# Performance work log

Hardware: AMD Instinct MI355X
Metric: run time of the kernel (lower is better)

## Reference

```python
import jax, jax.numpy as jnp
import numpy as np
from jax.scipy.special import erfc

# Problem scale
B, N, K = 16, 4000, 64          # systems, atoms/system, max neighbors
L = 30.0                         # cubic cell edge (Angstrom)
ALPHA = 0.3                      # Ewald splitting parameter (1/A), from config
KCUT = 1.0                       # reciprocal-space cutoff (1/A), from config
NMAX = 4                         # floor(KCUT / (2*pi/L)) -> static k-grid half-width
COULOMB_CONSTANT = 14.399645351950548  # e^2/(4 pi eps0) in eV*A


def setup_inputs() -> dict:
    key = jax.random.key(0)
    k1, k2, k3, k4 = jax.random.split(key, 4)
    T = B * N
    positions = jax.random.uniform(k1, (T, 3), dtype=jnp.float32) * L
    node_charges = jax.random.normal(k2, (T,), dtype=jnp.float32)
    cell = jnp.tile(jnp.eye(3, dtype=jnp.float32) * L, (B, 1, 1))
    # neighbor indices restricted to the same system; -1 marks self/padding
    local = jax.random.randint(k3, (T, K), 0, N)
    base = (jnp.arange(T) // N) * N
    nm = local + base[:, None]
    nm = jnp.where(nm == jnp.arange(T)[:, None], -1, nm).astype(jnp.int32)
    neighbor_shifts = jnp.zeros((T, K, 3), dtype=jnp.int32)
    num_neighbors = jnp.full((T,), K, dtype=jnp.int32)
    batch_idx = (jnp.arange(T) // N).astype(jnp.int32)
    return dict(positions=positions, node_charges=node_charges, cell=cell,
                neighbor_matrix=nm, neighbor_shifts=neighbor_shifts,
                num_neighbors=num_neighbors, batch_idx=batch_idx)


def _ewald_energies(positions, node_charges, cell, neighbor_matrix,
                    neighbor_shifts, num_neighbors, batch_idx):
    T = positions.shape[0]
    Bn = cell.shape[0]
    Nn = T // Bn
    Kn = neighbor_matrix.shape[1]
    q = node_charges.reshape(-1)
    dtype = positions.dtype
    alpha = jnp.full((Bn,), ALPHA, dtype=dtype)
    a_i = alpha[batch_idx]                                  # [T]

    # ---- real-space: neighbor gather + erfc + scatter-less per-atom sum ----
    mask = (neighbor_matrix >= 0) & (jnp.arange(Kn)[None, :] < num_neighbors[:, None])
    j = jnp.where(mask, neighbor_matrix, 0)                 # safe gather index [T,K]
    off = jnp.einsum('tks,tsd->tkd', neighbor_shifts.astype(dtype), cell[batch_idx])
    rij = positions[j] + off - positions[:, None, :]        # [T,K,3]
    d = jnp.sqrt(jnp.where(mask, jnp.sum(rij * rij, -1), 1.0))
    pair = jnp.where(mask, q[:, None] * q[j] * erfc(a_i[:, None] * d) / d, 0.0)
    # 0.5 for full (non-half) neighbor list; Gaussian self-interaction correction
    e_real = 0.5 * jnp.sum(pair, axis=-1) - a_i / jnp.sqrt(jnp.pi) * q * q  # [T]

    # ---- reciprocal-space: structure-factor sum over k-vectors ----
    rng = np.arange(-NMAX, NMAX + 1)
    nvec = np.stack(np.meshgrid(rng, rng, rng, indexing='ij'), -1).reshape(-1, 3)
    nvec = jnp.asarray(nvec, dtype=dtype)                   # [G,3] integer grid
    recip = 2.0 * jnp.pi * jnp.transpose(jnp.linalg.inv(cell), (0, 2, 1))  # rows b_j
    kv = jnp.einsum('gj,bjd->bgd', nvec, recip)             # [B,G,3]
    k2 = jnp.sum(kv * kv, -1)                               # [B,G]
    kmask = (k2 > 1e-10) & (k2 <= KCUT * KCUT)
    vol = jnp.abs(jnp.linalg.det(cell))                     # [B]
    a2 = alpha * alpha
    coef = jnp.where(kmask,
                     4.0 * jnp.pi * jnp.exp(-k2 / (4.0 * a2[:, None])) / jnp.where(kmask, k2, 1.0),
                     0.0) / (2.0 * vol[:, None])            # [B,G]
    pos_b = positions.reshape(Bn, Nn, 3)
    q_b = q.reshape(Bn, Nn)
    phase = jnp.einsum('bnd,bgd->bng', pos_b, kv)           # [B,N,G]
    c = jnp.cos(phase)
    s = jnp.sin(phase)
    Sre = jnp.einsum('bn,bng->bg', q_b, c)
    Sim = jnp.einsum('bn,bng->bg', q_b, s)
    e_recip = q_b * (jnp.einsum('bng,bg->bn', c, coef * Sre) +
                     jnp.einsum('bng,bg->bn', s, coef * Sim))  # [B,N]

    per_atom = e_real + e_recip.reshape(-1)
    energies = jax.ops.segment_sum(per_atom, batch_idx, num_segments=Bn)
    return energies * COULOMB_CONSTANT


def reference(positions, node_charges, cell, neighbor_matrix, neighbor_shifts,
              num_neighbors, batch_idx):
    return _ewald_energies(positions, node_charges, cell, neighbor_matrix,
                           neighbor_shifts, num_neighbors, batch_idx)
```

## Files before the change

### kernel.cpp

```cpp
#include <hip/hip_runtime.h>
#include <math.h>

#define GPB    8
#define GTOT   729
#define GMAX   46
#define KMAX   (GMAX*GPB)
#define APB    16
#define STRIDE 344

__device__ __forceinline__ float wave_reduce(float v) {
    #pragma unroll
    for (int off = 32; off > 0; off >>= 1) v += __shfl_down(v, off, 64);
    return v;
}

__device__ __forceinline__ float fast_erfc(float x) {
    float t = __builtin_amdgcn_rcpf(fmaf(0.3275911f, x, 1.0f));
    float p = fmaf(1.061405429f, t, -1.453152027f);
    p = fmaf(p, t, 1.421413741f);
    p = fmaf(p, t, -0.284496736f);
    p = fmaf(p, t, 0.254829592f);
    return p * t * __expf(-x * x);
}

__global__ __launch_bounds__(256)
void pack_pq(const float* __restrict__ pos, const float* __restrict__ chg,
             float4* __restrict__ pq, int T)
{
    int t = blockIdx.x * 256 + threadIdx.x;
    if (t < T)
        pq[t] = make_float4(pos[3*t], pos[3*t+1], pos[3*t+2], chg[t]);
}

__global__ __launch_bounds__(64)
void build_kvecs(const float* __restrict__ cell, float4* __restrict__ kcomp,
                 int* __restrict__ kcnt)
{
    const float TWO_PI = 6.283185307179586f;
    const float INV4A2 = 2.7777777777f;
    const float KC2    = 1.0f;

    int b    = blockIdx.x;
    int lane = threadIdx.x;

    const float* C = cell + 9 * b;
    float m00=C[0], m01=C[1], m02=C[2];
    float m10=C[3], m11=C[4], m12=C[5];
    float m20=C[6], m21=C[7], m22=C[8];
    float a00 = m11*m22 - m12*m21;
    float a01 = m02*m21 - m01*m22;
    float a02 = m01*m12 - m02*m11;
    float a10 = m12*m20 - m10*m22;
    float a11 = m00*m22 - m02*m20;
    float a12 = m02*m10 - m00*m12;
    float a20 = m10*m21 - m11*m20;
    float a21 = m01*m20 - m00*m21;
    float a22 = m00*m11 - m01*m10;
    float det = m00*a00 + m01*a10 + m02*a20;
    float invdet = 1.0f / det;
    float vol = fabsf(det);

    int cnt = 0;
    for (int base = 0; base < GTOT; base += 64) {
        int g = base + lane;
        float kx = 0.f, ky = 0.f, kz = 0.f, cf = 0.f;
        if (g < GTOT) {
            int ix = g / 81, rem = g - ix * 81;
            int iy = rem / 9, iz = rem - iy * 9;
            int nx = ix - 4, ny = iy - 4, nz = iz - 4;
            bool pos_half = (nx > 0) || (nx == 0 && (ny > 0 || (ny == 0 && nz > 0)));
            if (pos_half) {
                float fx = (float)nx, fy = (float)ny, fz = (float)nz;
                kx = TWO_PI * invdet * (fx*a00 + fy*a01 + fz*a02);
                ky = TWO_PI * invdet * (fx*a10 + fy*a11 + fz*a12);
                kz = TWO_PI * invdet * (fx*a20 + fy*a21 + fz*a22);
                float k2 = kx*kx + ky*ky + kz*kz;
                if (k2 > 1e-10f && k2 <= KC2) {
                    cf = 12.566370614359172f * __expf(-k2 * INV4A2) / (k2 * vol);
                }
            }
        }
        bool act = (cf != 0.f);
        unsigned long long m = __ballot(act);
        if (act) {
            int off = __popcll(m & ((1ull << lane) - 1ull));
            kcomp[b * KMAX + cnt + off] = make_float4(kx, ky, kz, cf);
        }
        cnt += (int)__popcll(m);
    }
    int padded = ((cnt + GPB - 1) / GPB) * GPB;
    if (lane < padded - cnt)
        kcomp[b * KMAX + cnt + lane] = make_float4(0.f, 0.f, 0.f, 0.f);
    if (lane == 0) kcnt[b] = padded / GPB;
}

__global__ __launch_bounds__(256)
void ewald_fused2(const float4* __restrict__ pq,
                  const float*  __restrict__ cell,
                  const int*    __restrict__ nm,
                  const int*    __restrict__ shifts,
                  const int*    __restrict__ nnb,
                  const float4* __restrict__ kcomp,
                  const int*    __restrict__ kcnt,
                  float* __restrict__ partial,
                  int T, int N, int K, int Bn, int CB)
{
    __shared__ float4 skv[GPB];
    __shared__ float  redA[4][GPB];
    __shared__ float  redB[4][GPB];
    __shared__ float  redr[4];

    const float ALPHA       = 0.3f;
    const float INV_SQRT_PI = 0.5641895835477563f;

    int blk  = blockIdx.x;
    int lane = threadIdx.x & 63;
    int w    = threadIdx.x >> 6;

    if (blk < CB) {
        int b    = blk / GMAX;
        int grp  = blk - b * GMAX;
        int slot = b * STRIDE + (N / APB) + grp;
        int ng   = kcnt[b];
        if (grp >= ng) {
            if (threadIdx.x == 0) partial[slot] = 0.f;
            return;
        }

        if (threadIdx.x < GPB)
            skv[threadIdx.x] = kcomp[b * KMAX + grp * GPB + threadIdx.x];
        __syncthreads();

        float kvx[GPB], kvy[GPB], kvz[GPB];
        #pragma unroll
        for (int gi = 0; gi < GPB; ++gi) {
            float4 v = skv[gi];
            kvx[gi] = v.x; kvy[gi] = v.y; kvz[gi] = v.z;
        }

        float Sre[GPB], Sim[GPB];
        #pragma unroll
        for (int gi = 0; gi < GPB; ++gi) { Sre[gi] = 0.f; Sim[gi] = 0.f; }

        const float4* pb = pq + (size_t)b * N;
        int a = threadIdx.x;
        for (; a + 256 < N; a += 512) {
            float4 v0 = pb[a];
            float4 v1 = pb[a + 256];
            #pragma unroll
            for (int gi = 0; gi < GPB; ++gi) {
                float ph0 = fmaf(v0.x, kvx[gi], fmaf(v0.y, kvy[gi], v0.z * kvz[gi]));
                float ph1 = fmaf(v1.x, kvx[gi], fmaf(v1.y, kvy[gi], v1.z * kvz[gi]));
                float s0, c0, s1, c1;
                __sincosf(ph0, &s0, &c0);
                __sincosf(ph1, &s1, &c1);
                Sre[gi] = fmaf(v0.w, c0, Sre[gi]);
                Sim[gi] = fmaf(v0.w, s0, Sim[gi]);
                Sre[gi] = fmaf(v1.w, c1, Sre[gi]);
                Sim[gi] = fmaf(v1.w, s1, Sim[gi]);
            }
        }
        if (a < N) {
            float4 v0 = pb[a];
            #pragma unroll
            for (int gi = 0; gi < GPB; ++gi) {
                float ph0 = fmaf(v0.x, kvx[gi], fmaf(v0.y, kvy[gi], v0.z * kvz[gi]));
                float s0, c0;
                __sincosf(ph0, &s0, &c0);
                Sre[gi] = fmaf(v0.w, c0, Sre[gi]);
                Sim[gi] = fmaf(v0.w, s0, Sim[gi]);
            }
        }

        #pragma unroll
        for (int gi = 0; gi < GPB; ++gi) {
            float sr = wave_reduce(Sre[gi]);
            float si = wave_reduce(Sim[gi]);
            if (lane == 0) { redA[w][gi] = sr; redB[w][gi] = si; }
        }
        __syncthreads();
        if (threadIdx.x < 64) {
            float e = 0.f;
            if (threadIdx.x < GPB) {
                int gi = threadIdx.x;
                float SR = redA[0][gi] + redA[1][gi] + redA[2][gi] + redA[3][gi];
                float SI = redB[0][gi] + redB[1][gi] + redB[2][gi] + redB[3][gi];
                e = skv[gi].w * (SR * SR + SI * SI);
            }
            e = wave_reduce(e);
            if (threadIdx.x == 0) partial[slot] = e;
        }
    } else {
        int rb = blk - CB;
        int t0 = rb * APB;
        int sys = t0 / N;

        float val = 0.0f;
        #pragma unroll
        for (int i = 0; i < APB/4; ++i) {
            int t = t0 + w * (APB/4) + i;
            float4 vi = pq[t];
            float xi = vi.x, yi = vi.y, zi = vi.z, qi = vi.w;
            if (lane == 0) val -= ALPHA * INV_SQRT_PI * qi * qi;
            int nn = nnb[t];
            for (int k = lane; k < K; k += 64) {
                int p = t * K + k;
                int j = nm[p];
                bool msk = (j >= 0) && (k < nn);
                if (msk) {
                    int sx = shifts[3*p], sy = shifts[3*p+1], sz = shifts[3*p+2];
                    float ox = 0.f, oy = 0.f, oz = 0.f;
                    if ((sx | sy | sz) != 0) {
                        const float* C = cell + 9 * sys;
                        float fx = (float)sx, fy = (float)sy, fz = (float)sz;
                        ox = fx*C[0] + fy*C[3] + fz*C[6];
                        oy = fx*C[1] + fy*C[4] + fz*C[7];
                        oz = fx*C[2] + fy*C[5] + fz*C[8];
                    }
                    float4 vj = pq[j];
                    float dx = vj.x + ox - xi;
                    float dy = vj.y + oy - yi;
                    float dz = vj.z + oz - zi;
                    float r2 = fmaf(dx, dx, fmaf(dy, dy, dz*dz));
                    float rinv = rsqrtf(r2);
                    float d = r2 * rinv;
                    val += 0.5f * qi * vj.w * fast_erfc(ALPHA * d) * rinv;
                }
            }
        }

        val = wave_reduce(val);
        if (lane == 0) redr[w] = val;
        __syncthreads();
        if (threadIdx.x == 0) {
            int rb_in_sys = rb - sys * (N / APB);
            partial[sys * STRIDE + rb_in_sys] =
                redr[0] + redr[1] + redr[2] + redr[3];
        }
    }
}

template <bool PACKED>
__global__ __launch_bounds__(256)
void ewald_fused(const float4* __restrict__ pq,
                 const float*  __restrict__ pos,
                 const float*  __restrict__ chg,
                 const float*  __restrict__ cell,
                 const int*    __restrict__ nm,
                 const int*    __restrict__ shifts,
                 const int*    __restrict__ nnb,
                 float* __restrict__ partial,
                 int T, int N, int K, int Bn, int CB)
{
    __shared__ float red[16];

    const float TWO_PI  = 6.283185307179586f;
    const float ALPHA   = 0.3f;
    const float INV4A2  = 2.7777777777f;
    const float KC2     = 1.0f;
    const float INV_SQRT_PI = 0.5641895835477563f;

    int blk = blockIdx.x;

    if (blk < CB) {
        int gpb_groups = (GTOT + GPB - 1) / GPB;
        int b   = blk / gpb_groups;
        int grp = blk % gpb_groups;

        const float* C = cell + 9 * b;
        float m00=C[0], m01=C[1], m02=C[2];
        float m10=C[3], m11=C[4], m12=C[5];
        float m20=C[6], m21=C[7], m22=C[8];
        float a00 = m11*m22 - m12*m21;
        float a01 = m02*m21 - m01*m22;
        float a02 = m01*m12 - m02*m11;
        float a10 = m12*m20 - m10*m22;
        float a11 = m00*m22 - m02*m20;
        float a12 = m02*m10 - m00*m12;
        float a20 = m10*m21 - m11*m20;
        float a21 = m01*m20 - m00*m21;
        float a22 = m00*m11 - m01*m10;
        float det = m00*a00 + m01*a10 + m02*a20;
        float invdet = 1.0f / det;
        float vol = fabsf(det);

        float kvx[GPB], kvy[GPB], kvz[GPB], coef[GPB];
        bool any = false;
        #pragma unroll
        for (int gi = 0; gi < GPB; ++gi) {
            int g = grp * GPB + gi;
            float cf = 0.f, kx = 0.f, ky = 0.f, kz = 0.f;
            if (g < GTOT) {
                int ix = g / 81, rem = g - ix * 81;
                int iy = rem / 9, iz = rem - iy * 9;
                int nx = ix - 4, ny = iy - 4, nz = iz - 4;
                bool pos_half = (nx > 0) || (nx == 0 && (ny > 0 || (ny == 0 && nz > 0)));
                if (pos_half) {
                    float fx = (float)nx, fy = (float)ny, fz = (float)nz;
                    kx = TWO_PI * invdet * (fx*a00 + fy*a01 + fz*a02);
                    ky = TWO_PI * invdet * (fx*a10 + fy*a11 + fz*a12);
                    kz = TWO_PI * invdet * (fx*a20 + fy*a21 + fz*a22);
                    float k2 = kx*kx + ky*ky + kz*kz;
                    if (k2 > 1e-10f && k2 <= KC2) {
                        cf = 12.566370614359172f * __expf(-k2 * INV4A2) / (k2 * vol);
                    }
                }
            }
            kvx[gi] = kx; kvy[gi] = ky; kvz[gi] = kz; coef[gi] = cf;
            any = any || (cf != 0.f);
        }

        int slot = b * STRIDE + (N / APB) + grp;
        if (!any) {
            if (threadIdx.x == 0) partial[slot] = 0.f;
            return;
        }

        float Sre[GPB], Sim[GPB];
        #pragma unroll
        for (int gi = 0; gi < GPB; ++gi) { Sre[gi] = 0.f; Sim[gi] = 0.f; }

        for (int a = threadIdx.x; a < N; a += 256) {
            float x, y, z, qa;
            if (PACKED) {
                float4 v = pq[(size_t)b * N + a];
                x = v.x; y = v.y; z = v.z; qa = v.w;
            } else {
                const float* pb = pos + (size_t)3 * (b * N + a);
                x = pb[0]; y = pb[1]; z = pb[2];
                qa = chg[(size_t)b * N + a];
            }
            #pragma unroll
            for (int gi = 0; gi < GPB; ++gi) {
                if (coef[gi] != 0.f) {
                    float ph = x*kvx[gi] + y*kvy[gi] + z*kvz[gi];
                    float s, c;
                    __sincosf(ph, &s, &c);
                    Sre[gi] = fmaf(qa, c, Sre[gi]);
                    Sim[gi] = fmaf(qa, s, Sim[gi]);
                }
            }
        }

        int lane = threadIdx.x & 63;
        int w    = threadIdx.x >> 6;
        float e_acc = 0.f;
        #pragma unroll
        for (int gi = 0; gi < GPB; ++gi) {
            if (coef[gi] != 0.f) {
                float sr = wave_reduce(Sre[gi]);
                float si = wave_reduce(Sim[gi]);
                if (lane == 0) { red[2*w] = sr; red[2*w+1] = si; }
                __syncthreads();
                if (threadIdx.x == 0) {
                    float SR = red[0] + red[2] + red[4] + red[6];
                    float SI = red[1] + red[3] + red[5] + red[7];
                    e_acc += coef[gi] * (SR*SR + SI*SI);
                }
                __syncthreads();
            }
        }
        if (threadIdx.x == 0) partial[slot] = e_acc;
    } else {
        int rb = blk - CB;
        int t0 = rb * APB;
        int sys = t0 / N;
        int lane = threadIdx.x & 63;
        int w    = threadIdx.x >> 6;

        float val = 0.0f;
        #pragma unroll
        for (int i = 0; i < APB/4; ++i) {
            int t = t0 + w * (APB/4) + i;
            float xi, yi, zi, qi;
            if (PACKED) {
                float4 v = pq[t];
                xi = v.x; yi = v.y; zi = v.z; qi = v.w;
            } else {
                xi = pos[3*t]; yi = pos[3*t+1]; zi = pos[3*t+2];
                qi = chg[t];
            }
            if (lane == 0) val -= ALPHA * INV_SQRT_PI * qi * qi;
            int nn = nnb[t];
            for (int k = lane; k < K; k += 64) {
                int p = t * K + k;
                int j = nm[p];
                bool msk = (j >= 0) && (k < nn);
                if (msk) {
                    int sx = shifts[3*p], sy = shifts[3*p+1], sz = shifts[3*p+2];
                    float ox = 0.f, oy = 0.f, oz = 0.f;
                    if ((sx | sy | sz) != 0) {
                        const float* C = cell + 9 * sys;
                        float fx = (float)sx, fy = (float)sy, fz = (float)sz;
                        ox = fx*C[0] + fy*C[3] + fz*C[6];
                        oy = fx*C[1] + fy*C[4] + fz*C[7];
                        oz = fx*C[2] + fy*C[5] + fz*C[8];
                    }
                    float xj, yj, zj, qj;
                    if (PACKED) {
                        float4 v = pq[j];
                        xj = v.x; yj = v.y; zj = v.z; qj = v.w;
                    } else {
                        xj = pos[3*j]; yj = pos[3*j+1]; zj = pos[3*j+2];
                        qj = chg[j];
                    }
                    float dx = xj + ox - xi;
                    float dy = yj + oy - yi;
                    float dz = zj + oz - zi;
                    float r2 = fmaf(dx, dx, fmaf(dy, dy, dz*dz));
                    float rinv = rsqrtf(r2);
                    float d = r2 * rinv;
                    val += 0.5f * qi * qj * erfcf(ALPHA * d) * rinv;
                }
            }
        }

        val = wave_reduce(val);
        if (lane == 0) red[w] = val;
        __syncthreads();
        if (threadIdx.x == 0) {
            int rb_in_sys = rb - sys * (N / APB);
            partial[sys * STRIDE + rb_in_sys] =
                red[0] + red[1] + red[2] + red[3];
        }
    }
}

__global__ __launch_bounds__(256)
void final_reduce(const float* __restrict__ partial, float* __restrict__ out,
                  int nslots)
{
    __shared__ float red[4];
    const float COUL = 14.399645351950548f;
    int b = blockIdx.x;
    float v = 0.f;
    for (int s = threadIdx.x; s < nslots; s += 256)
        v += partial[b * STRIDE + s];
    v = wave_reduce(v);
    int lane = threadIdx.x & 63, w = threadIdx.x >> 6;
    if (lane == 0) red[w] = v;
    __syncthreads();
    if (threadIdx.x == 0)
        out[b] = COUL * (red[0] + red[1] + red[2] + red[3]);
}

extern "C" void kernel_launch(void* const* d_in, const int* in_sizes, int n_in,
                              void* d_out, int out_size, void* d_ws, size_t ws_size,
                              hipStream_t stream) {
    const float* pos    = (const float*)d_in[0];
    const float* chg    = (const float*)d_in[1];
    const float* cellp  = (const float*)d_in[2];
    const int*   nm     = (const int*)d_in[3];
    const int*   shifts = (const int*)d_in[4];
    const int*   nnb    = (const int*)d_in[5];

    int T  = in_sizes[1];
    int Bn = in_sizes[2] / 9;
    int N  = T / Bn;
    int K  = in_sizes[3] / T;
    int RB = T / APB;

    size_t partBytes = (size_t)Bn * STRIDE * sizeof(float);
    size_t packOff   = ((partBytes + 255) / 256) * 256;
    size_t packBytes = (size_t)T * sizeof(float4);
    size_t kOff      = ((packOff + packBytes + 255) / 256) * 256;
    size_t kBytes    = (size_t)Bn * KMAX * sizeof(float4);
    size_t cntOff    = kOff + kBytes;
    size_t cntBytes  = (size_t)Bn * sizeof(int);

    float* partial = (float*)d_ws;

    if (ws_size >= cntOff + cntBytes) {
        float4* pq    = (float4*)((char*)d_ws + packOff);
        float4* kcomp = (float4*)((char*)d_ws + kOff);
        int*    kcnt  = (int*)((char*)d_ws + cntOff);
        int CB = Bn * GMAX;
        pack_pq<<<(T + 255) / 256, 256, 0, stream>>>(pos, chg, pq, T);
        build_kvecs<<<Bn, 64, 0, stream>>>(cellp, kcomp, kcnt);
        ewald_fused2<<<CB + RB, 256, 0, stream>>>(
            pq, cellp, nm, shifts, nnb, kcomp, kcnt, partial, T, N, K, Bn, CB);
        final_reduce<<<Bn, 256, 0, stream>>>(partial, (float*)d_out, N/APB + GMAX);
    } else {
        int CB = Bn * ((GTOT + GPB - 1) / GPB);
        int nslots = (N / APB) + ((GTOT + GPB - 1) / GPB);
        bool packed = (ws_size >= packOff + packBytes);
        if (packed) {
            float4* pq = (float4*)((char*)d_ws + packOff);
            pack_pq<<<(T + 255) / 256, 256, 0, stream>>>(pos, chg, pq, T);
            ewald_fused<true><<<CB + RB, 256, 0, stream>>>(
                pq, pos, chg, cellp, nm, shifts, nnb, partial, T, N, K, Bn, CB);
        } else {
            ewald_fused<false><<<CB + RB, 256, 0, stream>>>(
                nullptr, pos, chg, cellp, nm, shifts, nnb, partial, T, N, K, Bn, CB);
        }
        final_reduce<<<Bn, 256, 0, stream>>>(partial, (float*)d_out, nslots);
    }
}
```

Measured before the change: 128.6 us.

## Merge prologue kernels, fuse final reduction via atomic counter, enlarge real-space blocks

Merges pack_pq and build_kvecs into one prologue launch. The final_reduce kernel is removed: the last block per system, found through an atomic done counter, sums the partials and writes the output. Real-space blocks now cover 80 atoms instead of 16, K is specialized at compile time, and the neighbor loop becomes branchless with masked contributions. The aim is fewer launches and less per-block overhead, at the cost of atomics, a counter-reset dependency, and fewer real-space blocks.

Result: slower. 198.8 us (+54.6%).

```diff
diff --git a/kernel.cpp b/kernel.cpp
--- a/kernel.cpp
+++ b/kernel.cpp
@@ -5,8 +5,8 @@
 #define GTOT   729
 #define GMAX   46
 #define KMAX   (GMAX*GPB)
-#define APB    16
-#define STRIDE 344
+#define APB    80
+#define STRIDE_LEG 344
 
 __device__ __forceinline__ float wave_reduce(float v) {
     #pragma unroll
@@ -24,23 +24,25 @@
 }
 
 __global__ __launch_bounds__(256)
-void pack_pq(const float* __restrict__ pos, const float* __restrict__ chg,
-             float4* __restrict__ pq, int T)
+void prologue(const float* __restrict__ pos, const float* __restrict__ chg,
+              float4* __restrict__ pq, const float* __restrict__ cell,
+              float4* __restrict__ kcomp, int* __restrict__ kcnt,
+              int* __restrict__ done, int T, int PB)
 {
-    int t = blockIdx.x * 256 + threadIdx.x;
-    if (t < T)
-        pq[t] = make_float4(pos[3*t], pos[3*t+1], pos[3*t+2], chg[t]);
-}
-
-__global__ __launch_bounds__(64)
-void build_kvecs(const float* __restrict__ cell, float4* __restrict__ kcomp,
-                 int* __restrict__ kcnt)
-{
+    int blk = blockIdx.x;
+    if (blk < PB) {
+        int t = blk * 256 + threadIdx.x;
+        if (t < T)
+            pq[t] = make_float4(pos[3*t], pos[3*t+1], pos[3*t+2], chg[t]);
+        return;
+    }
+    int b = blk - PB;
+    if (threadIdx.x == 64) done[b] = 0;
+    if (threadIdx.x >= 64) return;
+
     const float TWO_PI = 6.283185307179586f;
     const float INV4A2 = 2.7777777777f;
     const float KC2    = 1.0f;
-
-    int b    = blockIdx.x;
     int lane = threadIdx.x;
 
     const float* C = cell + 9 * b;
@@ -94,179 +96,198 @@
     if (lane == 0) kcnt[b] = padded / GPB;
 }
 
+template <int KK>
 __global__ __launch_bounds__(256)
-void ewald_fused2(const float4* __restrict__ pq,
-                  const float*  __restrict__ cell,
-                  const int*    __restrict__ nm,
-                  const int*    __restrict__ shifts,
-                  const int*    __restrict__ nnb,
-                  const float4* __restrict__ kcomp,
-                  const int*    __restrict__ kcnt,
-                  float* __restrict__ partial,
-                  int T, int N, int K, int Bn, int CB)
+void ewald_main(const float4* __restrict__ pq,
+                const float*  __restrict__ cell,
+                const int*    __restrict__ nm,
+                const int*    __restrict__ shifts,
+                const int*    __restrict__ nnb,
+                const float4* __restrict__ kcomp,
+                const int*    __restrict__ kcnt,
+                float* __restrict__ partial,
+                int*   __restrict__ done,
+                float* __restrict__ out,
+                int T, int N, int K, int Bn, int CB, int RPS)
 {
     __shared__ float4 skv[GPB];
     __shared__ float  redA[4][GPB];
     __shared__ float  redB[4][GPB];
     __shared__ float  redr[4];
+    __shared__ float  redf[4];
+    __shared__ int    sflag;
 
     const float ALPHA       = 0.3f;
     const float INV_SQRT_PI = 0.5641895835477563f;
 
     int blk  = blockIdx.x;
-    int lane = threadIdx.x & 63;
-    int w    = threadIdx.x >> 6;
+    int tid  = threadIdx.x;
+    int lane = tid & 63;
+    int w    = tid >> 6;
+    int stride = RPS + GMAX;
+
+    float pval = 0.f;
+    int sys, slot;
 
     if (blk < CB) {
-        int b    = blk / GMAX;
-        int grp  = blk - b * GMAX;
-        int slot = b * STRIDE + (N / APB) + grp;
-        int ng   = kcnt[b];
-        if (grp >= ng) {
-            if (threadIdx.x == 0) partial[slot] = 0.f;
-            return;
-        }
-
-        if (threadIdx.x < GPB)
-            skv[threadIdx.x] = kcomp[b * KMAX + grp * GPB + threadIdx.x];
-        __syncthreads();
-
-        float kvx[GPB], kvy[GPB], kvz[GPB];
-        #pragma unroll
-        for (int gi = 0; gi < GPB; ++gi) {
-            float4 v = skv[gi];
-            kvx[gi] = v.x; kvy[gi] = v.y; kvz[gi] = v.z;
-        }
-
-        float Sre[GPB], Sim[GPB];
-        #pragma unroll
-        for (int gi = 0; gi < GPB; ++gi) { Sre[gi] = 0.f; Sim[gi] = 0.f; }
-
-        const float4* pb = pq + (size_t)b * N;
-        int a = threadIdx.x;
-        for (; a + 256 < N; a += 512) {
-            float4 v0 = pb[a];
-            float4 v1 = pb[a + 256];
+        int b   = blk / GMAX;
+        int grp = blk - b * GMAX;
+        sys  = b;
+        slot = b * stride + RPS + grp;
+        int ng = kcnt[b];
+
+        if (grp < ng) {
+            if (tid < GPB)
+                skv[tid] = kcomp[b * KMAX + grp * GPB + tid];
+            __syncthreads();
+
+            float kvx[GPB], kvy[GPB], kvz[GPB];
             #pragma unroll
             for (int gi = 0; gi < GPB; ++gi) {
-                float ph0 = fmaf(v0.x, kvx[gi], fmaf(v0.y, kvy[gi], v0.z * kvz[gi]));
-                float ph1 = fmaf(v1.x, kvx[gi], fmaf(v1.y, kvy[gi], v1.z * kvz[gi]));
-                float s0, c0, s1, c1;
-                __sincosf(ph0, &s0, &c0);
-                __sincosf(ph1, &s1, &c1);
-                Sre[gi] = fmaf(v0.w, c0, Sre[gi]);
-                Sim[gi] = fmaf(v0.w, s0, Sim[gi]);
-                Sre[gi] = fmaf(v1.w, c1, Sre[gi]);
-                Sim[gi] = fmaf(v1.w, s1, Sim[gi]);
-            }
-        }
-        if (a < N) {
-            float4 v0 = pb[a];
+                float4 v = skv[gi];
+                kvx[gi] = v.x; kvy[gi] = v.y; kvz[gi] = v.z;
+            }
+
+            float Sre[GPB], Sim[GPB];
+            #pragma unroll
+            for (int gi = 0; gi < GPB; ++gi) { Sre[gi] = 0.f; Sim[gi] = 0.f; }
+
+            const float4* pb = pq + (size_t)b * N;
+            int a = tid;
+            for (; a + 256 < N; a += 512) {
+                float4 v0 = pb[a];
+                float4 v1 = pb[a + 256];
+                #pragma unroll
+                for (int gi = 0; gi < GPB; ++gi) {
+                    float ph0 = fmaf(v0.x, kvx[gi], fmaf(v0.y, kvy[gi], v0.z * kvz[gi]));
+                    float ph1 = fmaf(v1.x, kvx[gi], fmaf(v1.y, kvy[gi], v1.z * kvz[gi]));
+                    float s0, c0, s1, c1;
+                    __sincosf(ph0, &s0, &c0);
+                    __sincosf(ph1, &s1, &c1);
+                    Sre[gi] = fmaf(v0.w, c0, Sre[gi]);
+                    Sim[gi] = fmaf(v0.w, s0, Sim[gi]);
+                    Sre[gi] = fmaf(v1.w, c1, Sre[gi]);
+                    Sim[gi] = fmaf(v1.w, s1, Sim[gi]);
+                }
+            }
+            if (a < N) {
+                float4 v0 = pb[a];
+                #pragma unroll
+                for (int gi = 0; gi < GPB; ++gi) {
+                    float ph0 = fmaf(v0.x, kvx[gi], fmaf(v0.y, kvy[gi], v0.z * kvz[gi]));
+                    float s0, c0;
+                    __sincosf(ph0, &s0, &c0);
+                    Sre[gi] = fmaf(v0.w, c0, Sre[gi]);
+                    Sim[gi] = fmaf(v0.w, s0, Sim[gi]);
+                }
+            }
+
             #pragma unroll
             for (int gi = 0; gi < GPB; ++gi) {
-                float ph0 = fmaf(v0.x, kvx[gi], fmaf(v0.y, kvy[gi], v0.z * kvz[gi]));
-                float s0, c0;
-                __sincosf(ph0, &s0, &c0);
-                Sre[gi] = fmaf(v0.w, c0, Sre[gi]);
-                Sim[gi] = fmaf(v0.w, s0, Sim[gi]);
-            }
-        }
-
-        #pragma unroll
-        for (int gi = 0; gi < GPB; ++gi) {
-            float sr = wave_reduce(Sre[gi]);
-            float si = wave_reduce(Sim[gi]);
-            if (lane == 0) { redA[w][gi] = sr; redB[w][gi] = si; }
-        }
-        __syncthreads();
-        if (threadIdx.x < 64) {
-            float e = 0.f;
-            if (threadIdx.x < GPB) {
-                int gi = threadIdx.x;
-                float SR = redA[0][gi] + redA[1][gi] + redA[2][gi] + redA[3][gi];
-                float SI = redB[0][gi] + redB[1][gi] + redB[2][gi] + redB[3][gi];
-                e = skv[gi].w * (SR * SR + SI * SI);
-            }
-            e = wave_reduce(e);
-            if (threadIdx.x == 0) partial[slot] = e;
+                float sr = wave_reduce(Sre[gi]);
+                float si = wave_reduce(Sim[gi]);
+                if (lane == 0) { redA[w][gi] = sr; redB[w][gi] = si; }
+            }
+            __syncthreads();
+            if (tid < 64) {
+                float e = 0.f;
+                if (tid < GPB) {
+                    float SR = redA[0][tid] + redA[1][tid] + redA[2][tid] + redA[3][tid];
+                    float SI = redB[0][tid] + redB[1][tid] + redB[2][tid] + redB[3][tid];
+                    e = skv[tid].w * (SR * SR + SI * SI);
+                }
+                pval = wave_reduce(e);
+            }
         }
     } else {
         int rb = blk - CB;
         int t0 = rb * APB;
-        int sys = t0 / N;
+        sys  = t0 / N;
+        slot = sys * stride + (rb - sys * RPS);
+        const int Keff = KK ? KK : K;
+        const float* C = cell + 9 * sys;
 
         float val = 0.0f;
-        #pragma unroll
+        #pragma unroll 4
         for (int i = 0; i < APB/4; ++i) {
             int t = t0 + w * (APB/4) + i;
             float4 vi = pq[t];
-            float xi = vi.x, yi = vi.y, zi = vi.z, qi = vi.w;
-            if (lane == 0) val -= ALPHA * INV_SQRT_PI * qi * qi;
+            float xi = vi.x, yi = vi.y, zi = vi.z;
+            float hqi = 0.5f * vi.w;
+            if (lane == 0) val -= ALPHA * INV_SQRT_PI * vi.w * vi.w;
             int nn = nnb[t];
-            for (int k = lane; k < K; k += 64) {
-                int p = t * K + k;
+            for (int k = lane; k < Keff; k += 64) {
+                int p = t * Keff + k;
                 int j = nm[p];
                 bool msk = (j >= 0) && (k < nn);
-                if (msk) {
-                    int sx = shifts[3*p], sy = shifts[3*p+1], sz = shifts[3*p+2];
-                    float ox = 0.f, oy = 0.f, oz = 0.f;
-                    if ((sx | sy | sz) != 0) {
-                        const float* C = cell + 9 * sys;
-                        float fx = (float)sx, fy = (float)sy, fz = (float)sz;
-                        ox = fx*C[0] + fy*C[3] + fz*C[6];
-                        oy = fx*C[1] + fy*C[4] + fz*C[7];
-                        oz = fx*C[2] + fy*C[5] + fz*C[8];
-                    }
-                    float4 vj = pq[j];
-                    float dx = vj.x + ox - xi;
-                    float dy = vj.y + oy - yi;
-                    float dz = vj.z + oz - zi;
-                    float r2 = fmaf(dx, dx, fmaf(dy, dy, dz*dz));
-                    float rinv = rsqrtf(r2);
-                    float d = r2 * rinv;
-                    val += 0.5f * qi * vj.w * fast_erfc(ALPHA * d) * rinv;
-                }
+                int js = j < 0 ? 0 : j;
+                int sx = shifts[3*p], sy = shifts[3*p+1], sz = shifts[3*p+2];
+                float4 vj = pq[js];
+                float ox = 0.f, oy = 0.f, oz = 0.f;
+                if ((sx | sy | sz) != 0) {
+                    float fx = (float)sx, fy = (float)sy, fz = (float)sz;
+                    ox = fx*C[0] + fy*C[3] + fz*C[6];
+                    oy = fx*C[1] + fy*C[4] + fz*C[7];
+                    oz = fx*C[2] + fy*C[5] + fz*C[8];
+                }
+                float dx = vj.x + ox - xi;
+                float dy = vj.y + oy - yi;
+                float dz = vj.z + oz - zi;
+                float r2 = fmaf(dx, dx, fmaf(dy, dy, dz*dz));
+                r2 = msk ? r2 : 1.0f;
+                float rinv = rsqrtf(r2);
+                float d = r2 * rinv;
+                float e = fast_erfc(ALPHA * d);
+                float c = msk ? hqi * vj.w : 0.f;
+                val = fmaf(c * rinv, e, val);
             }
         }
 
         val = wave_reduce(val);
         if (lane == 0) redr[w] = val;
         __syncthreads();
-        if (threadIdx.x == 0) {
-            int rb_in_sys = rb - sys * (N / APB);
-            partial[sys * STRIDE + rb_in_sys] =
-                redr[0] + redr[1] + redr[2] + redr[3];
-        }
-    }
-}
-
-template <bool PACKED>
+        if (tid == 0) pval = redr[0] + redr[1] + redr[2] + redr[3];
+    }
+
+    if (tid == 0) {
+        __hip_atomic_store(&partial[slot], pval, __ATOMIC_RELEASE,
+                           __HIP_MEMORY_SCOPE_AGENT);
+        int old = __hip_atomic_fetch_add(&done[sys], 1, __ATOMIC_ACQ_REL,
+                                         __HIP_MEMORY_SCOPE_AGENT);
+        sflag = (old == stride - 1);
+    }
+    __syncthreads();
+    if (sflag) {
+        float v = 0.f;
+        for (int s = tid; s < stride; s += 256)
+            v += __hip_atomic_load(&partial[sys * stride + s], __ATOMIC_RELAXED,
+                                   __HIP_MEMORY_SCOPE_AGENT);
+        v = wave_reduce(v);
+        if (lane == 0) redf[w] = v;
+        __syncthreads();
+        if (tid == 0)
+            out[sys] = 14.399645351950548f * (redf[0] + redf[1] + redf[2] + redf[3]);
+    }
+}
+
 __global__ __launch_bounds__(256)
-void ewald_fused(const float4* __restrict__ pq,
-                 const float*  __restrict__ pos,
-                 const float*  __restrict__ chg,
-                 const float*  __restrict__ cell,
-                 const int*    __restrict__ nm,
-                 const int*    __restrict__ shifts,
-                 const int*    __restrict__ nnb,
-                 float* __restrict__ partial,
-                 int T, int N, int K, int Bn, int CB)
+void ewald_legacy(const float* __restrict__ pos, const float* __restrict__ chg,
+                  const float* __restrict__ cell, const int* __restrict__ nm,
+                  const int* __restrict__ shifts, const int* __restrict__ nnb,
+                  float* __restrict__ partial, int T, int N, int K, int Bn, int CB)
 {
     __shared__ float red[16];
-
     const float TWO_PI  = 6.283185307179586f;
     const float ALPHA   = 0.3f;
     const float INV4A2  = 2.7777777777f;
     const float KC2     = 1.0f;
     const float INV_SQRT_PI = 0.5641895835477563f;
-
     int blk = blockIdx.x;
 
     if (blk < CB) {
         int gpb_groups = (GTOT + GPB - 1) / GPB;
         int b   = blk / gpb_groups;
         int grp = blk % gpb_groups;
-
         const float* C = cell + 9 * b;
         float m00=C[0], m01=C[1], m02=C[2];
         float m10=C[3], m11=C[4], m12=C[5];
@@ -301,35 +322,23 @@
                     ky = TWO_PI * invdet * (fx*a10 + fy*a11 + fz*a12);
                     kz = TWO_PI * invdet * (fx*a20 + fy*a21 + fz*a22);
                     float k2 = kx*kx + ky*ky + kz*kz;
-                    if (k2 > 1e-10f && k2 <= KC2) {
+                    if (k2 > 1e-10f && k2 <= KC2)
                         cf = 12.566370614359172f * __expf(-k2 * INV4A2) / (k2 * vol);
-                    }
                 }
             }
             kvx[gi] = kx; kvy[gi] = ky; kvz[gi] = kz; coef[gi] = cf;
             any = any || (cf != 0.f);
         }
-
-        int slot = b * STRIDE + (N / APB) + grp;
-        if (!any) {
-            if (threadIdx.x == 0) partial[slot] = 0.f;
-            return;
-        }
+        int slot = b * STRIDE_LEG + (N / 16) + grp;
+        if (!any) { if (threadIdx.x == 0) partial[slot] = 0.f; return; }
 
         float Sre[GPB], Sim[GPB];
         #pragma unroll
         for (int gi = 0; gi < GPB; ++gi) { Sre[gi] = 0.f; Sim[gi] = 0.f; }
-
         for (int a = threadIdx.x; a < N; a += 256) {
-            float x, y, z, qa;
-            if (PACKED) {
-                float4 v = pq[(size_t)b * N + a];
-                x = v.x; y = v.y; z = v.z; qa = v.w;
-            } else {
-                const float* pb = pos + (size_t)3 * (b * N + a);
-                x = pb[0]; y = pb[1]; z = pb[2];
-                qa = chg[(size_t)b * N + a];
-            }
+            const float* pp = pos + (size_t)3 * (b * N + a);
+            float x = pp[0], y = pp[1], z = pp[2];
+            float qa = chg[(size_t)b * N + a];
             #pragma unroll
             for (int gi = 0; gi < GPB; ++gi) {
                 if (coef[gi] != 0.f) {
@@ -341,9 +350,7 @@
                 }
             }
         }
-
-        int lane = threadIdx.x & 63;
-        int w    = threadIdx.x >> 6;
+        int lane = threadIdx.x & 63, w = threadIdx.x >> 6;
         float e_acc = 0.f;
         #pragma unroll
         for (int gi = 0; gi < GPB; ++gi) {
@@ -363,23 +370,15 @@
         if (threadIdx.x == 0) partial[slot] = e_acc;
     } else {
         int rb = blk - CB;
-        int t0 = rb * APB;
+        int t0 = rb * 16;
         int sys = t0 / N;
-        int lane = threadIdx.x & 63;
-        int w    = threadIdx.x >> 6;
-
+        int lane = threadIdx.x & 63, w = threadIdx.x >> 6;
         float val = 0.0f;
         #pragma unroll
-        for (int i = 0; i < APB/4; ++i) {
-            int t = t0 + w * (APB/4) + i;
-            float xi, yi, zi, qi;
-            if (PACKED) {
-                float4 v = pq[t];
-                xi = v.x; yi = v.y; zi = v.z; qi = v.w;
-            } else {
-                xi = pos[3*t]; yi = pos[3*t+1]; zi = pos[3*t+2];
-                qi = chg[t];
-            }
+        for (int i = 0; i < 4; ++i) {
+            int t = t0 + w * 4 + i;
+            float xi = pos[3*t], yi = pos[3*t+1], zi = pos[3*t+2];
+            float qi = chg[t];
             if (lane == 0) val -= ALPHA * INV_SQRT_PI * qi * qi;
             int nn = nnb[t];
             for (int k = lane; k < K; k += 64) {
@@ -396,46 +395,36 @@
                         oy = fx*C[1] + fy*C[4] + fz*C[7];
                         oz = fx*C[2] + fy*C[5] + fz*C[8];
                     }
-                    float xj, yj, zj, qj;
-                    if (PACKED) {
-                        float4 v = pq[j];
-                        xj = v.x; yj = v.y; zj = v.z; qj = v.w;
-                    } else {
-                        xj = pos[3*j]; yj = pos[3*j+1]; zj = pos[3*j+2];
-                        qj = chg[j];
-                    }
-                    float dx = xj + ox - xi;
-                    float dy = yj + oy - yi;
-                    float dz = zj + oz - zi;
+                    float dx = pos[3*j] + ox - xi;
+                    float dy = pos[3*j+1] + oy - yi;
+                    float dz = pos[3*j+2] + oz - zi;
                     float r2 = fmaf(dx, dx, fmaf(dy, dy, dz*dz));
                     float rinv = rsqrtf(r2);
                     float d = r2 * rinv;
-                    val += 0.5f * qi * qj * erfcf(ALPHA * d) * rinv;
-                }
-            }
-        }
-
+                    val += 0.5f * qi * chg[j] * fast_erfc(ALPHA * d) * rinv;
+                }
+            }
+        }
         val = wave_reduce(val);
         if (lane == 0) red[w] = val;
         __syncthreads();
         if (threadIdx.x == 0) {
-            int rb_in_sys = rb - sys * (N / APB);
-            partial[sys * STRIDE + rb_in_sys] =
-                red[0] + red[1] + red[2] + red[3];
+            int rb_in_sys = rb - sys * (N / 16);
+            partial[sys * STRIDE_LEG + rb_in_sys] = red[0] + red[1] + red[2] + red[3];
         }
     }
 }
 
 __global__ __launch_bounds__(256)
 void final_reduce(const float* __restrict__ partial, float* __restrict__ out,
-                  int nslots)
+                  int nslots, int stride)
 {
     __shared__ float red[4];
     const float COUL = 14.399645351950548f;
     int b = blockIdx.x;
     float v = 0.f;
     for (int s = threadIdx.x; s < nslots; s += 256)
-        v += partial[b * STRIDE + s];
+        v += partial[b * stride + s];
     v = wave_reduce(v);
     int lane = threadIdx.x & 63, w = threadIdx.x >> 6;
     if (lane == 0) red[w] = v;
@@ -458,41 +447,47 @@
     int Bn = in_sizes[2] / 9;
     int N  = T / Bn;
     int K  = in_sizes[3] / T;
-    int RB = T / APB;
-
-    size_t partBytes = (size_t)Bn * STRIDE * sizeof(float);
-    size_t packOff   = ((partBytes + 255) / 256) * 256;
-    size_t packBytes = (size_t)T * sizeof(float4);
-    size_t kOff      = ((packOff + packBytes + 255) / 256) * 256;
+
+    int RPS = N / APB;
+    int stride = RPS + GMAX;
+    size_t partBytes = (size_t)Bn * stride * sizeof(float);
+    size_t pqOff     = ((partBytes + 255) / 256) * 256;
+    size_t pqBytes   = (size_t)T * sizeof(float4);
+    size_t kOff      = ((pqOff + pqBytes + 255) / 256) * 256;
     size_t kBytes    = (size_t)Bn * KMAX * sizeof(float4);
     size_t cntOff    = kOff + kBytes;
-    size_t cntBytes  = (size_t)Bn * sizeof(int);
-
-    float* partial = (float*)d_ws;
-
-    if (ws_size >= cntOff + cntBytes) {
-        float4* pq    = (float4*)((char*)d_ws + packOff);
-        float4* kcomp = (float4*)((char*)d_ws + kOff);
-        int*    kcnt  = (int*)((char*)d_ws + cntOff);
+    size_t doneOff   = cntOff + ((size_t)Bn * sizeof(int) + 63) / 64 * 64;
+    size_t needed    = doneOff + (size_t)Bn * sizeof(int);
+
+    if ((N % APB) == 0 && ws_size >= needed) {
+        float*  partial = (float*)d_ws;
+        float4* pq      = (float4*)((char*)d_ws + pqOff);
+        float4* kcomp   = (float4*)((char*)d_ws + kOff);
+        int*    kcnt    = (int*)((char*)d_ws + cntOff);
+        int*    done    = (int*)((char*)d_ws + doneOff);
+
+        int PB = (T + 255) / 256;
         int CB = Bn * GMAX;
-        pack_pq<<<(T + 255) / 256, 256, 0, stream>>>(pos, chg, pq, T);
-        build_kvecs<<<Bn, 64, 0, stream>>>(cellp, kcomp, kcnt);
-        ewald_fused2<<<CB + RB, 256, 0, stream>>>(
-            pq, cellp, nm, shifts, nnb, kcomp, kcnt, partial, T, N, K, Bn, CB);
-        final_reduce<<<Bn, 256, 0, stream>>>(partial, (float*)d_out, N/APB + GMAX);
+        int RB = T / APB;
+
+        prologue<<<PB + Bn, 256, 0, stream>>>(pos, chg, pq, cellp, kcomp, kcnt,
+                                              done, T, PB);
+        if (K == 64)
+            ewald_main<64><<<CB + RB, 256, 0, stream>>>(
+                pq, cellp, nm, shifts, nnb, kcomp, kcnt, partial, done,
+                (float*)d_out, T, N, K, Bn, CB, RPS);
+        else
+            ewald_main<0><<<CB + RB, 256, 0, stream>>>(
+                pq, cellp, nm, shifts, nnb, kcomp, kcnt, partial, done,
+                (float*)d_out, T, N, K, Bn, CB, RPS);
     } else {
+        float* partial = (float*)d_ws;
         int CB = Bn * ((GTOT + GPB - 1) / GPB);
-        int nslots = (N / APB) + ((GTOT + GPB - 1) / GPB);
-        bool packed = (ws_size >= packOff + packBytes);
-        if (packed) {
-            float4* pq = (float4*)((char*)d_ws + packOff);
-            pack_pq<<<(T + 255) / 256, 256, 0, stream>>>(pos, chg, pq, T);
-            ewald_fused<true><<<CB + RB, 256, 0, stream>>>(
-                pq, pos, chg, cellp, nm, shifts, nnb, partial, T, N, K, Bn, CB);
-        } else {
-            ewald_fused<false><<<CB + RB, 256, 0, stream>>>(
-                nullptr, pos, chg, cellp, nm, shifts, nnb, partial, T, N, K, Bn, CB);
-        }
-        final_reduce<<<Bn, 256, 0, stream>>>(partial, (float*)d_out, nslots);
-    }
-}
+        int RB = T / 16;
+        int nslots = (N / 16) + ((GTOT + GPB - 1) / GPB);
+        ewald_legacy<<<CB + RB, 256, 0, stream>>>(pos, chg, cellp, nm, shifts,
+                                                  nnb, partial, T, N, K, Bn, CB);
+        final_reduce<<<Bn, 256, 0, stream>>>(partial, (float*)d_out, nslots,
+                                             STRIDE_LEG);
+    }
+}
```
